# Optimization experiments

Measured on AMD Instinct MI355X. Metric: run time of the kernel, lower is better.

## Reference

```python
import jax, jax.numpy as jnp
import numpy as np

HALF = 16  # num_outputs // 2 with num_features = 32
EPS = 1e-5


def _gmul(Wm, h):
    # Wm: [B,N,M,J], h: [B,M,F] -> [B,N,J*F] (j-major feature layout, matching torch split/cat/bmm)
    B, N = Wm.shape[0], Wm.shape[1]
    return jnp.einsum('bnmj,bmf->bnjf', Wm, h).reshape(B, N, -1)


def _bn(z, g, b):
    # training-mode BatchNorm2d on [R, C, 1, 1] == per-channel norm over rows, biased var
    m = z.mean(axis=0)
    v = z.var(axis=0)
    return g * (z - m) / jnp.sqrt(v + EPS) + b


def _block(W, hx, W_lg, hy, P, wx2x, wy2x, bx, wy2y, wx2y, by, gx, btx, gy, bty):
    B, N, M = P.shape[0], P.shape[1], P.shape[2]
    x2x = _gmul(W, hx).reshape(-1, wx2x.shape[0])
    y2x = _gmul(P, hy).reshape(-1, wy2x.shape[0])
    zx = x2x @ wx2x + y2x @ wy2x + bx
    zx = jnp.concatenate([jax.nn.relu(zx[:, :HALF]), zx[:, HALF:]], axis=1)
    xo = _bn(zx, gx, btx).reshape(B, N, -1)
    y2y = _gmul(W_lg, hy).reshape(-1, wy2y.shape[0])
    x2y = _gmul(jnp.swapaxes(P, 1, 2), hx).reshape(-1, wx2y.shape[0])
    zy = y2y @ wy2y + x2y @ wx2y + by
    zy = jnp.concatenate([jax.nn.relu(zy[:, :HALF]), zy[:, HALF:]], axis=1)
    yo = _bn(zy, gy, bty).reshape(B, M, -1)
    return xo, yo


def _forward(W, x, W_lg, y, P,
             wx2x0, wy2x0, bx0, wy2y0, wx2y0, by0, gx0, btx0, gy0, bty0,
             wx2x_m, wy2x_m, bx_m, wy2y_m, wx2y_m, by_m, gx_m, btx_m, gy_m, bty_m,
             wlx, wly, bl):
    hx, hy = _block(W, x, W_lg, y, P, wx2x0, wy2x0, bx0, wy2y0, wx2y0, by0,
                    gx0, btx0, gy0, bty0)
    for i in range(wx2x_m.shape[0]):  # fixed num_layers loop
        hx, hy = _block(W, hx, W_lg, hy, P,
                        wx2x_m[i], wy2x_m[i], bx_m[i], wy2y_m[i], wx2y_m[i], by_m[i],
                        gx_m[i], btx_m[i], gy_m[i], bty_m[i])
    # final layer: linear only, x branch output
    x2x = _gmul(W, hx).reshape(-1, wlx.shape[0])
    y2x = _gmul(P, hy).reshape(-1, wly.shape[0])
    out = (x2x @ wlx + y2x @ wly + bl).reshape(W.shape[0], W.shape[1], -1)
    return out


def setup_inputs() -> dict:
    key = jax.random.key(0)
    ks = iter(jax.random.split(key, 40))
    B, N, M, J, F, L, C = 1, 2048, 4096, 3, 32, 6, 2
    d = {}
    d['W'] = jax.random.normal(next(ks), (B, N, N, J), jnp.float32)
    d['x'] = jax.random.normal(next(ks), (B, N, 1), jnp.float32)
    d['W_lg'] = jax.random.normal(next(ks), (B, M, M, J), jnp.float32)
    d['y'] = jax.random.normal(next(ks), (B, M, 1), jnp.float32)
    d['P'] = jax.random.normal(next(ks), (B, N, M, 2), jnp.float32)
    s = 0.1
    d['wx2x0'] = jax.random.normal(next(ks), (J * 1, F), jnp.float32) * s
    d['wy2x0'] = jax.random.normal(next(ks), (2 * 1, F), jnp.float32) * s
    d['bx0'] = jax.random.normal(next(ks), (F,), jnp.float32) * s
    d['wy2y0'] = jax.random.normal(next(ks), (J * 1, F), jnp.float32) * s
    d['wx2y0'] = jax.random.normal(next(ks), (2 * 1, F), jnp.float32) * s
    d['by0'] = jax.random.normal(next(ks), (F,), jnp.float32) * s
    d['gx0'] = jnp.ones((F,), jnp.float32)
    d['btx0'] = jnp.zeros((F,), jnp.float32)
    d['gy0'] = jnp.ones((F,), jnp.float32)
    d['bty0'] = jnp.zeros((F,), jnp.float32)
    d['wx2x_m'] = jax.random.normal(next(ks), (L, J * F, F), jnp.float32) * s
    d['wy2x_m'] = jax.random.normal(next(ks), (L, 2 * F, F), jnp.float32) * s
    d['bx_m'] = jax.random.normal(next(ks), (L, F), jnp.float32) * s
    d['wy2y_m'] = jax.random.normal(next(ks), (L, J * F, F), jnp.float32) * s
    d['wx2y_m'] = jax.random.normal(next(ks), (L, 2 * F, F), jnp.float32) * s
    d['by_m'] = jax.random.normal(next(ks), (L, F), jnp.float32) * s
    d['gx_m'] = jnp.ones((L, F), jnp.float32)
    d['btx_m'] = jnp.zeros((L, F), jnp.float32)
    d['gy_m'] = jnp.ones((L, F), jnp.float32)
    d['bty_m'] = jnp.zeros((L, F), jnp.float32)
    d['wlx'] = jax.random.normal(next(ks), (J * F, C), jnp.float32) * s
    d['wly'] = jax.random.normal(next(ks), (2 * F, C), jnp.float32) * s
    d['bl'] = jax.random.normal(next(ks), (C,), jnp.float32) * s
    return d


def reference(W, x, W_lg, y, P,
              wx2x0, wy2x0, bx0, wy2y0, wx2y0, by0, gx0, btx0, gy0, bty0,
              wx2x_m, wy2x_m, bx_m, wy2y_m, wx2y_m, by_m, gx_m, btx_m, gy_m, bty_m,
              wlx, wly, bl):
    return _forward(W, x, W_lg, y, P,
                    wx2x0, wy2x0, bx0, wy2y0, wx2y0, by0, gx0, btx0, gy0, bty0,
                    wx2x_m, wy2x_m, bx_m, wy2y_m, wx2y_m, by_m, gx_m, btx_m, gy_m, bty_m,
                    wlx, wly, bl)
```

## Files before the change

### kernel.cpp

```cpp
#include <hip/hip_runtime.h>

typedef _Float16 f16x8 __attribute__((ext_vector_type(8)));
typedef float f32x4 __attribute__((ext_vector_type(4)));


__device__ inline unsigned short f16b(float v) {
    _Float16 h = (_Float16)v;
    return __builtin_bit_cast(unsigned short, h);
}

__device__ inline void atomAddF(float* p, float v) {
    __hip_atomic_fetch_add(p, v, __ATOMIC_RELAXED, __HIP_MEMORY_SCOPE_AGENT);
}

template<int K>
__device__ inline void pack_cvt4(const float* __restrict__ src, unsigned short* __restrict__ dst, int q) {
    const int KSTEPS = K / 32;
    int r15 = q & 15;
    int blk = q >> 4;
    int panel = blk / KSTEPS;
    int kstep = blk - panel * KSTEPS;
    int row = (panel << 4) | r15;
    const float4* s = (const float4*)(src + (size_t)row * K + (kstep << 5));
    uint4* d = (uint4*)dst;
    #pragma unroll
    for (int g = 0; g < 4; ++g) {
        float4 v0 = s[g * 2], v1 = s[g * 2 + 1];
        uint4 qq;
        qq.x = (unsigned)f16b(v0.x) | ((unsigned)f16b(v0.y) << 16);
        qq.y = (unsigned)f16b(v0.z) | ((unsigned)f16b(v0.w) << 16);
        qq.z = (unsigned)f16b(v1.x) | ((unsigned)f16b(v1.y) << 16);
        qq.w = (unsigned)f16b(v1.z) | ((unsigned)f16b(v1.w) << 16);
        d[(size_t)blk * 64 + g * 16 + r15] = qq;
    }
}

__device__ inline void build_one(int t2,
    const float* __restrict__ srcx, const float* __restrict__ srcy,
    int Fin, int Fout, int buildB2, int use_bn,
    const float* __restrict__ stats,
    const float* __restrict__ w1a, const float* __restrict__ w1b,
    const float* __restrict__ w2a, const float* __restrict__ w2b,
    unsigned short* __restrict__ B1f, unsigned short* __restrict__ B2f) {
    const int NB1 = 14336 * 32;
    int isB2 = 0;
    if (t2 >= NB1) {
        if (!buildB2) return;
        isB2 = 1; t2 -= NB1;
        if (t2 >= 16384 * 32) return;
    }
    int g = t2 & 31;
    int k = t2 >> 5;
    float v = 0.f;
    if (g < Fout) {
        const float* hr; const float* wc; int useY;
        if (!isB2) {
            if (k < 6144) { int m = k / 3, j = k - 3 * m; hr = srcx + m * Fin; wc = w1a + (j * Fin) * Fout + g; useY = 0; }
            else { int k2 = k - 6144; int m = k2 >> 1, p = k2 & 1; hr = srcy + m * Fin; wc = w1b + (p * Fin) * Fout + g; useY = 1; }
        } else {
            if (k < 12288) { int m = k / 3, j = k - 3 * m; hr = srcy + m * Fin; wc = w2a + (j * Fin) * Fout + g; useY = 1; }
            else { int k2 = k - 12288; int n = k2 >> 1, p = k2 & 1; hr = srcx + n * Fin; wc = w2b + (p * Fin) * Fout + g; useY = 0; }
        }
        float a = 0.f;
        if (use_bn) {
            const float* sc = useY ? stats + 196 : stats + 132;
            const float* sh = useY ? stats + 228 : stats + 164;
            #pragma unroll
            for (int f = 0; f < 32; ++f) {
                float h = sc[f] * hr[f] + sh[f];
                a += h * wc[f * Fout];
            }
        } else {
            for (int f = 0; f < Fin; ++f) a += hr[f] * wc[f * Fout];
        }
        v = a;
    }
    int e = k & 7, kw = (k >> 3) & 3, t = k >> 5, hh = g >> 4;
    int off = (((t * 2 + hh) * 64 + (kw << 4) + (g & 15)) << 3) | e;
    if (!isB2) B1f[off] = f16b(v); else B2f[off] = f16b(v);
}

__global__ __launch_bounds__(256) void prep(const float* __restrict__ W, const float* __restrict__ WL,
                                            const float* __restrict__ P,
                                            const float* __restrict__ x, const float* __restrict__ y,
                                            const float* __restrict__ wx2x0, const float* __restrict__ wy2x0,
                                            const float* __restrict__ wy2y0, const float* __restrict__ wx2y0,
                                            unsigned short* __restrict__ Wb, unsigned short* __restrict__ WLb,
                                            unsigned short* __restrict__ Pb, unsigned short* __restrict__ PT,
                                            unsigned short* __restrict__ B1f, unsigned short* __restrict__ B2f) {
    __shared__ unsigned int lds[64][33];
    int bid = blockIdx.x;
    int tid = threadIdx.x;
    if (bid < 2048) {
        const int QW = 393216, QTOT = 393216 + 1572864;
        for (int q = bid * 256 + tid; q < QTOT; q += 2048 * 256) {
            if (q < QW) pack_cvt4<6144>(W, Wb, q);
            else pack_cvt4<12288>(WL, WLb, q - QW);
        }
        return;
    }
    if (bid >= 6144) {
        build_one((bid - 6144) * 256 + tid, x, y, 1, 32, 1, 0, nullptr,
                  wx2x0, wy2x0, wy2y0, wx2y0, B1f, B2f);
        return;
    }
    int vb = bid - 2048;
    int m0 = (vb & 127) * 32;
    int n0 = (vb >> 7) * 64;
    const float2* P2 = (const float2*)P;
    #pragma unroll
    for (int it = 0; it < 8; ++it) {
        int idx = it * 256 + tid;
        int nl = idx >> 5, ml = idx & 31;
        float2 v = P2[(size_t)(n0 + nl) * 4096 + (m0 + ml)];
        unsigned int pk = (unsigned int)f16b(v.x) | ((unsigned int)f16b(v.y) << 16);
        lds[nl][ml] = pk;
    }
    __syncthreads();
    uint4* PT4 = (uint4*)PT;
    uint4* Pb4 = (uint4*)Pb;
    #pragma unroll
    for (int it = 0; it < 2; ++it) {
        int t2 = it * 256 + tid;
        {
            int r15 = t2 & 15, kw = (t2 >> 4) & 3, ksi = (t2 >> 6) & 3, pi = t2 >> 8;
            int ml = pi * 16 + r15;
            int nl0 = ksi * 16 + kw * 4;
            uint4 u;
            u.x = lds[nl0][ml]; u.y = lds[nl0 + 1][ml]; u.z = lds[nl0 + 2][ml]; u.w = lds[nl0 + 3][ml];
            int rowp = (m0 >> 4) + pi;
            int ks = (n0 >> 4) + ksi;
            PT4[(size_t)rowp * 8192 + ks * 64 + kw * 16 + r15] = u;
        }
        {
            int r15 = t2 & 15, kw = (t2 >> 4) & 3, ksi = (t2 >> 6) & 1, pi = t2 >> 7;
            int nl = pi * 16 + r15;
            int ml0 = ksi * 16 + kw * 4;
            uint4 u;
            u.x = lds[nl][ml0]; u.y = lds[nl][ml0 + 1]; u.z = lds[nl][ml0 + 2]; u.w = lds[nl][ml0 + 3];
            int rowp = (n0 >> 4) + pi;
            int ks = (m0 >> 4) + ksi;
            Pb4[(size_t)rowp * 16384 + ks * 64 + kw * 16 + r15] = u;
        }
    }
}

__global__ __launch_bounds__(256) void build_b(
    const float* __restrict__ srcx, const float* __restrict__ srcy,
    int Fin, int Fout, int buildB2, int use_bn,
    const float* __restrict__ stats,
    const float* __restrict__ w1a, const float* __restrict__ w1b,
    const float* __restrict__ w2a, const float* __restrict__ w2b,
    unsigned short* __restrict__ B1f, unsigned short* __restrict__ B2f) {
    build_one(blockIdx.x * 256 + threadIdx.x, srcx, srcy, Fin, Fout, buildB2, use_bn,
              stats, w1a, w1b, w2a, w2b, B1f, B2f);
}

__global__ __launch_bounds__(256) void gemm_k(
    const unsigned short* __restrict__ Wb, const unsigned short* __restrict__ Pb,
    const unsigned short* __restrict__ WLb, const unsigned short* __restrict__ PTb,
    const unsigned short* __restrict__ B1f, const unsigned short* __restrict__ B2f,
    float* __restrict__ px, float* __restrict__ py, float* __restrict__ stats, int nwgx) {
    __shared__ float lds[4][1024];
    int bid = blockIdx.x;
    if (bid == 0 && threadIdx.x < 132) stats[threadIdx.x] = 0.f;
    const unsigned short* Bf;
    float* Z;
    int seg, Mbase, K, kloc, kb;
    const unsigned short* A16;
    if (bid < nwgx) {
        Bf = B1f;
        int mwg = bid / 14; seg = bid % 14;
        Mbase = mwg * 32;
        kb = seg << 10;
        Z = px + (size_t)seg * 65536;
        if (seg < 6) { K = 6144; kloc = kb;        A16 = Wb; }
        else         { K = 8192; kloc = kb - 6144; A16 = Pb; }
    } else {
        int b2 = bid - nwgx;
        Bf = B2f;
        int mwg = b2 / 16; seg = b2 % 16;
        Mbase = mwg * 32;
        kb = seg << 10;
        Z = py + (size_t)seg * 131072;
        if (seg < 12) { K = 12288; kloc = kb;         A16 = WLb; }
        else          { K = 4096;  kloc = kb - 12288; A16 = PTb; }
    }
    int wid = threadIdx.x >> 6, lane = threadIdx.x & 63;
    int kq = wid << 8;
    const unsigned short* ap0 = A16 + (size_t)(Mbase >> 4) * (K * 16)
                              + (size_t)((kloc + kq) >> 5) * 512 + lane * 8;
    const unsigned short* ap1 = ap0 + (size_t)K * 16;
    const unsigned short* bp = Bf + ((size_t)((kb + kq) >> 5)) * 1024 + lane * 8;
    f32x4 acc00 = {0.f,0.f,0.f,0.f}, acc01 = {0.f,0.f,0.f,0.f};
    f32x4 acc10 = {0.f,0.f,0.f,0.f}, acc11 = {0.f,0.f,0.f,0.f};
    #pragma unroll
    for (int ks = 0; ks < 8; ++ks) {
        f16x8 a0 = *(const f16x8*)ap0;
        f16x8 a1 = *(const f16x8*)ap1;
        f16x8 b0 = *(const f16x8*)bp;
        f16x8 b1 = *(const f16x8*)(bp + 512);
        acc00 = __builtin_amdgcn_mfma_f32_16x16x32_f16(a0, b0, acc00, 0, 0, 0);
        acc10 = __builtin_amdgcn_mfma_f32_16x16x32_f16(a1, b0, acc10, 0, 0, 0);
        acc01 = __builtin_amdgcn_mfma_f32_16x16x32_f16(a0, b1, acc01, 0, 0, 0);
        acc11 = __builtin_amdgcn_mfma_f32_16x16x32_f16(a1, b1, acc11, 0, 0, 0);
        ap0 += 512; ap1 += 512; bp += 1024;
    }
    int col = lane & 15, r0 = (lane >> 4) << 2;
    float* l = lds[wid];
    #pragma unroll
    for (int r = 0; r < 4; ++r) {
        l[(r0 + r) * 32 + col]            = acc00[r];
        l[(r0 + r) * 32 + col + 16]       = acc01[r];
        l[(r0 + r + 16) * 32 + col]       = acc10[r];
        l[(r0 + r + 16) * 32 + col + 16]  = acc11[r];
    }
    __syncthreads();
    int t = threadIdx.x;
    float4 a = ((const float4*)lds[0])[t];
    float4 b = ((const float4*)lds[1])[t];
    float4 c = ((const float4*)lds[2])[t];
    float4 d = ((const float4*)lds[3])[t];
    float4 s;
    s.x = (a.x + b.x) + (c.x + d.x);
    s.y = (a.y + b.y) + (c.y + d.y);
    s.z = (a.z + b.z) + (c.z + d.z);
    s.w = (a.w + b.w) + (c.w + d.w);
    ((float4*)(Z + (size_t)Mbase * 32))[t] = s;
}

__global__ __launch_bounds__(256) void reduce_stats(
    const float* __restrict__ px, const float* __restrict__ py,
    const float* __restrict__ bx, const float* __restrict__ by,
    const float* __restrict__ gx, const float* __restrict__ btx,
    const float* __restrict__ gy, const float* __restrict__ bty,
    float* __restrict__ zax, float* __restrict__ zay,
    float* __restrict__ stats) {
    __shared__ float lsum[4][8][8];
    __shared__ int lastFlag;
    int bid = blockIdx.x, tid = threadIdx.x;
    const float4* src; const float* bias; float4* dst; float* st; int nseg, i4, stride4;
    if (bid < 64) { src = (const float4*)px; bias = bx; dst = (float4*)zax; st = stats;      nseg = 14; i4 = bid * 256 + tid;        stride4 = 16384; }
    else          { src = (const float4*)py; bias = by; dst = (float4*)zay; st = stats + 64; nseg = 16; i4 = (bid - 64) * 256 + tid; stride4 = 32768; }
    float4 s = {0.f, 0.f, 0.f, 0.f};
    for (int g = 0; g < nseg; ++g) {
        float4 v = src[(size_t)g * stride4 + i4];
        s.x += v.x; s.y += v.y; s.z += v.z; s.w += v.w;
    }
    int c0 = (i4 & 7) * 4;
    float4 b4 = *(const float4*)(bias + c0);
    s.x += b4.x; s.y += b4.y; s.z += b4.z; s.w += b4.w;
    if (c0 < 16) {
        s.x = fmaxf(s.x, 0.f); s.y = fmaxf(s.y, 0.f);
        s.z = fmaxf(s.z, 0.f); s.w = fmaxf(s.w, 0.f);
    }
    dst[i4] = s;
    float4 s2 = {s.x * s.x, s.y * s.y, s.z * s.z, s.w * s.w};
    #pragma unroll
    for (int mask = 8; mask <= 32; mask <<= 1) {
        s.x += __shfl_xor(s.x, mask); s.y += __shfl_xor(s.y, mask);
        s.z += __shfl_xor(s.z, mask); s.w += __shfl_xor(s.w, mask);
        s2.x += __shfl_xor(s2.x, mask); s2.y += __shfl_xor(s2.y, mask);
        s2.z += __shfl_xor(s2.z, mask); s2.w += __shfl_xor(s2.w, mask);
    }
    int w = tid >> 6, ln = tid & 63;
    if (ln < 8) {
        lsum[w][ln][0] = s.x;  lsum[w][ln][1] = s.y;  lsum[w][ln][2] = s.z;  lsum[w][ln][3] = s.w;
        lsum[w][ln][4] = s2.x; lsum[w][ln][5] = s2.y; lsum[w][ln][6] = s2.z; lsum[w][ln][7] = s2.w;
    }
    __syncthreads();
    if (tid < 64) {
        int q = tid >> 3, e = tid & 7;
        float v = lsum[0][q][e] + lsum[1][q][e] + lsum[2][q][e] + lsum[3][q][e];
        int col = q * 4 + (e & 3);
        atomAddF((e < 4) ? &st[col] : &st[32 + col], v);
    }
    __syncthreads();
    if (tid == 0) {
        __threadfence();
        int old = __hip_atomic_fetch_add((int*)(stats + 128), 1, __ATOMIC_ACQ_REL, __HIP_MEMORY_SCOPE_AGENT);
        lastFlag = (old == 191) ? 1 : 0;
    }
    __syncthreads();
    if (lastFlag && tid < 64) {
        int f = tid & 31, isY = tid >> 5;
        float* sb = stats + (isY ? 64 : 0);
        float n = isY ? 4096.f : 2048.f;
        float sum = __hip_atomic_load(&sb[f], __ATOMIC_RELAXED, __HIP_MEMORY_SCOPE_AGENT);
        float ssq = __hip_atomic_load(&sb[32 + f], __ATOMIC_RELAXED, __HIP_MEMORY_SCOPE_AGENT);
        float mean = sum / n;
        float var = ssq / n - mean * mean;
        const float* gv = isY ? gy : gx;
        const float* bv = isY ? bty : btx;
        float sc = gv[f] * rsqrtf(var + 1e-5f);
        stats[132 + isY * 64 + f] = sc;
        stats[164 + isY * 64 + f] = bv[f] - mean * sc;
    }
}

__global__ __launch_bounds__(256) void out_final(const float* __restrict__ px,
                                                 const float* __restrict__ bl,
                                                 float* __restrict__ out) {
    int tid = blockIdx.x * 256 + threadIdx.x;
    if (tid < 4096) {
        int n = tid >> 1, c = tid & 1;
        float a = bl[c];
        for (int s = 0; s < 14; ++s) a += px[(size_t)s * 65536 + n * 32 + c];
        out[tid] = a;
    }
}

extern "C" void kernel_launch(void* const* d_in, const int* in_sizes, int n_in,
                              void* d_out, int out_size, void* d_ws, size_t ws_size,
                              hipStream_t stream) {
    const float* W    = (const float*)d_in[0];
    const float* x    = (const float*)d_in[1];
    const float* WL   = (const float*)d_in[2];
    const float* y    = (const float*)d_in[3];
    const float* P    = (const float*)d_in[4];
    const float* wx2x0 = (const float*)d_in[5];
    const float* wy2x0 = (const float*)d_in[6];
    const float* bx0   = (const float*)d_in[7];
    const float* wy2y0 = (const float*)d_in[8];
    const float* wx2y0 = (const float*)d_in[9];
    const float* by0   = (const float*)d_in[10];
    const float* gx0   = (const float*)d_in[11];
    const float* btx0  = (const float*)d_in[12];
    const float* gy0   = (const float*)d_in[13];
    const float* bty0  = (const float*)d_in[14];
    const float* wx2x_m = (const float*)d_in[15];
    const float* wy2x_m = (const float*)d_in[16];
    const float* bx_m   = (const float*)d_in[17];
    const float* wy2y_m = (const float*)d_in[18];
    const float* wx2y_m = (const float*)d_in[19];
    const float* by_m   = (const float*)d_in[20];
    const float* gx_m   = (const float*)d_in[21];
    const float* btx_m  = (const float*)d_in[22];
    const float* gy_m   = (const float*)d_in[23];
    const float* bty_m  = (const float*)d_in[24];
    const float* wlx = (const float*)d_in[25];
    const float* wly = (const float*)d_in[26];
    const float* bl  = (const float*)d_in[27];

    char* base = (char*)d_ws;
    unsigned short* Wb  = (unsigned short*)(base + 0);
    unsigned short* Pb  = (unsigned short*)(base + 25165824);
    unsigned short* WLb = (unsigned short*)(base + 58720256);
    unsigned short* PTb = (unsigned short*)(base + 159383552);
    unsigned short* B1f = (unsigned short*)(base + 192937984);
    unsigned short* B2f = (unsigned short*)(base + 193855488);
    float* zax   = (float*)(base + 194904064);
    float* zay   = (float*)(base + 195166208);
    float* stats = (float*)(base + 195690496);
    float* px    = (float*)(base + 195692544);
    float* py    = (float*)(base + 199362560);

    prep<<<9984, 256, 0, stream>>>(W, WL, P, x, y, wx2x0, wy2x0, wy2y0, wx2y0,
                                   Wb, WLb, Pb, PTb, B1f, B2f);

    gemm_k<<<2944, 256, 0, stream>>>(Wb, Pb, WLb, PTb, B1f, B2f, px, py, stats, 896);
    reduce_stats<<<192, 256, 0, stream>>>(px, py, bx0, by0, gx0, btx0, gy0, bty0, zax, zay, stats);

    for (int i = 0; i < 6; ++i) {
        build_b<<<3840, 256, 0, stream>>>(zax, zay, 32, 32, 1, 1, stats,
                                          wx2x_m + i * 3072, wy2x_m + i * 2048,
                                          wy2y_m + i * 3072, wx2y_m + i * 2048, B1f, B2f);
        gemm_k<<<2944, 256, 0, stream>>>(Wb, Pb, WLb, PTb, B1f, B2f, px, py, stats, 896);
        reduce_stats<<<192, 256, 0, stream>>>(px, py, bx_m + i * 32, by_m + i * 32,
                                              gx_m + i * 32, btx_m + i * 32,
                                              gy_m + i * 32, bty_m + i * 32, zax, zay, stats);
    }

    build_b<<<1792, 256, 0, stream>>>(zax, zay, 32, 2, 0, 1, stats,
                                      wlx, wly, nullptr, nullptr, B1f, B2f);
    gemm_k<<<896, 256, 0, stream>>>(Wb, Pb, WLb, PTb, B1f, B2f, px, py, stats, 896);
    out_final<<<16, 256, 0, stream>>>(px, bl, (float*)d_out);
}
```

Before: 602.7 us.

## Stage W/WL fp16 packing through LDS and software-pipeline GEMM operand loads

The fp32-to-fp16 packing of W and W_lg into MFMA panel layout now reads coalesced rows into a padded LDS tile, then writes packed 16-byte chunks. Previously each thread gathered strided 128-byte row segments. This targets uncoalesced global reads in the prep kernel, which streams the largest tensors. Separately, the GEMM inner loop now prefetches the next k-step's A/B fragments before issuing the current MFMAs, hiding load latency at the cost of extra registers.

```diff
diff --git a/kernel.cpp b/kernel.cpp
--- a/kernel.cpp
+++ b/kernel.cpp
@@ -2,7 +2,10 @@
 
 typedef _Float16 f16x8 __attribute__((ext_vector_type(8)));
 typedef float f32x4 __attribute__((ext_vector_type(4)));
-
+typedef unsigned short us4v __attribute__((ext_vector_type(4)));
+
+
+#define LPITCH 1036
 
 __device__ inline unsigned short f16b(float v) {
     _Float16 h = (_Float16)v;
@@ -14,24 +17,29 @@
 }
 
 template<int K>
-__device__ inline void pack_cvt4(const float* __restrict__ src, unsigned short* __restrict__ dst, int q) {
-    const int KSTEPS = K / 32;
-    int r15 = q & 15;
-    int blk = q >> 4;
-    int panel = blk / KSTEPS;
-    int kstep = blk - panel * KSTEPS;
-    int row = (panel << 4) | r15;
-    const float4* s = (const float4*)(src + (size_t)row * K + (kstep << 5));
-    uint4* d = (uint4*)dst;
-    #pragma unroll
-    for (int g = 0; g < 4; ++g) {
-        float4 v0 = s[g * 2], v1 = s[g * 2 + 1];
-        uint4 qq;
-        qq.x = (unsigned)f16b(v0.x) | ((unsigned)f16b(v0.y) << 16);
-        qq.y = (unsigned)f16b(v0.z) | ((unsigned)f16b(v0.w) << 16);
-        qq.z = (unsigned)f16b(v1.x) | ((unsigned)f16b(v1.y) << 16);
-        qq.w = (unsigned)f16b(v1.z) | ((unsigned)f16b(v1.w) << 16);
-        d[(size_t)blk * 64 + g * 16 + r15] = qq;
+__device__ inline void cvt_tile(const float* __restrict__ src, unsigned short* __restrict__ dst,
+                                int panel, int t0, unsigned short* lbuf) {
+    int tid = threadIdx.x;
+    int w = tid >> 6, lane = tid & 63;
+    const float* base = src + (size_t)(panel * 16) * K + t0 * 1024;
+    #pragma unroll 4
+    for (int i = 0; i < 16; ++i) {
+        float4 v = *((const float4*)(base + (size_t)i * K + w * 256) + lane);
+        us4v h;
+        h[0] = f16b(v.x); h[1] = f16b(v.y); h[2] = f16b(v.z); h[3] = f16b(v.w);
+        *(us4v*)(lbuf + i * LPITCH + w * 256 + lane * 4) = h;
+    }
+    __syncthreads();
+    uint4* d = (uint4*)dst + (size_t)panel * (K * 2) + t0 * 2048;
+    #pragma unroll
+    for (int j = 0; j < 8; ++j) {
+        int u = j * 256 + tid;
+        int r15 = u & 15, g = (u >> 4) & 3, ksl = u >> 6;
+        const unsigned short* p = lbuf + r15 * LPITCH + ksl * 32 + g * 8;
+        uint2 lo = *(const uint2*)p;
+        uint2 hi = *(const uint2*)(p + 4);
+        uint4 q; q.x = lo.x; q.y = lo.y; q.z = hi.x; q.w = hi.y;
+        d[u] = q;
     }
 }
 
@@ -88,23 +96,22 @@
                                             unsigned short* __restrict__ Wb, unsigned short* __restrict__ WLb,
                                             unsigned short* __restrict__ Pb, unsigned short* __restrict__ PT,
                                             unsigned short* __restrict__ B1f, unsigned short* __restrict__ B2f) {
-    __shared__ unsigned int lds[64][33];
+    __shared__ __align__(16) unsigned char smem[16 * LPITCH * 2];
     int bid = blockIdx.x;
     int tid = threadIdx.x;
-    if (bid < 2048) {
-        const int QW = 393216, QTOT = 393216 + 1572864;
-        for (int q = bid * 256 + tid; q < QTOT; q += 2048 * 256) {
-            if (q < QW) pack_cvt4<6144>(W, Wb, q);
-            else pack_cvt4<12288>(WL, WLb, q - QW);
-        }
+    if (bid < 3840) {
+        unsigned short* lbuf = (unsigned short*)smem;
+        if (bid < 768) cvt_tile<6144>(W, Wb, bid / 6, bid % 6, lbuf);
+        else { int b = bid - 768; cvt_tile<12288>(WL, WLb, b / 12, b % 12, lbuf); }
         return;
     }
-    if (bid >= 6144) {
-        build_one((bid - 6144) * 256 + tid, x, y, 1, 32, 1, 0, nullptr,
+    if (bid >= 7936) {
+        build_one((bid - 7936) * 256 + tid, x, y, 1, 32, 1, 0, nullptr,
                   wx2x0, wy2x0, wy2y0, wx2y0, B1f, B2f);
         return;
     }
-    int vb = bid - 2048;
+    unsigned int (*lds)[33] = (unsigned int (*)[33])smem;
+    int vb = bid - 3840;
     int m0 = (vb & 127) * 32;
     int n0 = (vb >> 7) * 64;
     const float2* P2 = (const float2*)P;
@@ -194,18 +201,27 @@
     const unsigned short* bp = Bf + ((size_t)((kb + kq) >> 5)) * 1024 + lane * 8;
     f32x4 acc00 = {0.f,0.f,0.f,0.f}, acc01 = {0.f,0.f,0.f,0.f};
     f32x4 acc10 = {0.f,0.f,0.f,0.f}, acc11 = {0.f,0.f,0.f,0.f};
-    #pragma unroll
-    for (int ks = 0; ks < 8; ++ks) {
-        f16x8 a0 = *(const f16x8*)ap0;
-        f16x8 a1 = *(const f16x8*)ap1;
-        f16x8 b0 = *(const f16x8*)bp;
-        f16x8 b1 = *(const f16x8*)(bp + 512);
+    f16x8 a0 = *(const f16x8*)ap0;
+    f16x8 a1 = *(const f16x8*)ap1;
+    f16x8 b0 = *(const f16x8*)bp;
+    f16x8 b1 = *(const f16x8*)(bp + 512);
+    #pragma unroll
+    for (int ks = 0; ks < 7; ++ks) {
+        ap0 += 512; ap1 += 512; bp += 1024;
+        f16x8 na0 = *(const f16x8*)ap0;
+        f16x8 na1 = *(const f16x8*)ap1;
+        f16x8 nb0 = *(const f16x8*)bp;
+        f16x8 nb1 = *(const f16x8*)(bp + 512);
         acc00 = __builtin_amdgcn_mfma_f32_16x16x32_f16(a0, b0, acc00, 0, 0, 0);
         acc10 = __builtin_amdgcn_mfma_f32_16x16x32_f16(a1, b0, acc10, 0, 0, 0);
         acc01 = __builtin_amdgcn_mfma_f32_16x16x32_f16(a0, b1, acc01, 0, 0, 0);
         acc11 = __builtin_amdgcn_mfma_f32_16x16x32_f16(a1, b1, acc11, 0, 0, 0);
-        ap0 += 512; ap1 += 512; bp += 1024;
-    }
+        a0 = na0; a1 = na1; b0 = nb0; b1 = nb1;
+    }
+    acc00 = __builtin_amdgcn_mfma_f32_16x16x32_f16(a0, b0, acc00, 0, 0, 0);
+    acc10 = __builtin_amdgcn_mfma_f32_16x16x32_f16(a1, b0, acc10, 0, 0, 0);
+    acc01 = __builtin_amdgcn_mfma_f32_16x16x32_f16(a0, b1, acc01, 0, 0, 0);
+    acc11 = __builtin_amdgcn_mfma_f32_16x16x32_f16(a1, b1, acc11, 0, 0, 0);
     int col = lane & 15, r0 = (lane >> 4) << 2;
     float* l = lds[wid];
     #pragma unroll
@@ -355,8 +371,8 @@
     float* px    = (float*)(base + 195692544);
     float* py    = (float*)(base + 199362560);
 
-    prep<<<9984, 256, 0, stream>>>(W, WL, P, x, y, wx2x0, wy2x0, wy2y0, wx2y0,
-                                   Wb, WLb, Pb, PTb, B1f, B2f);
+    prep<<<11776, 256, 0, stream>>>(W, WL, P, x, y, wx2x0, wy2x0, wy2y0, wx2y0,
+                                    Wb, WLb, Pb, PTb, B1f, B2f);
 
     gemm_k<<<2944, 256, 0, stream>>>(Wb, Pb, WLb, PTb, B1f, B2f, px, py, stats, 896);
     reduce_stats<<<192, 256, 0, stream>>>(px, py, bx0, by0, gx0, btx0, gy0, bty0, zax, zay, stats);
```

After: 590.0 us (median of 2 runs). -2.1%, faster.

## Split GEMM waves by row panel and K-half with register double-buffered loads

Applied to the files above, without the earlier changes.

Each workgroup's four waves are re-partitioned: instead of every wave covering both 16-row panels over a quarter of K, each wave now owns one row panel over half of K, running 16 k-steps with two accumulators instead of 8 steps with four. Global loads are double-buffered in registers so the next step's A/B fragments are fetched while the current MFMAs issue. The LDS reduction drops from a 4-way to a 2-way sum and the LDS footprint is halved. In exchange, each wave reloads B fragments that were previously shared across the two panels, which raises B traffic, and the per-wave dependency chain is longer.

```diff
diff --git a/kernel.cpp b/kernel.cpp
--- a/kernel.cpp
+++ b/kernel.cpp
@@ -161,7 +161,7 @@
     const unsigned short* __restrict__ WLb, const unsigned short* __restrict__ PTb,
     const unsigned short* __restrict__ B1f, const unsigned short* __restrict__ B2f,
     float* __restrict__ px, float* __restrict__ py, float* __restrict__ stats, int nwgx) {
-    __shared__ float lds[4][1024];
+    __shared__ float lds[4][512];
     int bid = blockIdx.x;
     if (bid == 0 && threadIdx.x < 132) stats[threadIdx.x] = 0.f;
     const unsigned short* Bf;
@@ -187,45 +187,46 @@
         else          { K = 4096;  kloc = kb - 12288; A16 = PTb; }
     }
     int wid = threadIdx.x >> 6, lane = threadIdx.x & 63;
-    int kq = wid << 8;
-    const unsigned short* ap0 = A16 + (size_t)(Mbase >> 4) * (K * 16)
-                              + (size_t)((kloc + kq) >> 5) * 512 + lane * 8;
-    const unsigned short* ap1 = ap0 + (size_t)K * 16;
-    const unsigned short* bp = Bf + ((size_t)((kb + kq) >> 5)) * 1024 + lane * 8;
-    f32x4 acc00 = {0.f,0.f,0.f,0.f}, acc01 = {0.f,0.f,0.f,0.f};
-    f32x4 acc10 = {0.f,0.f,0.f,0.f}, acc11 = {0.f,0.f,0.f,0.f};
-    #pragma unroll
-    for (int ks = 0; ks < 8; ++ks) {
-        f16x8 a0 = *(const f16x8*)ap0;
-        f16x8 a1 = *(const f16x8*)ap1;
-        f16x8 b0 = *(const f16x8*)bp;
-        f16x8 b1 = *(const f16x8*)(bp + 512);
-        acc00 = __builtin_amdgcn_mfma_f32_16x16x32_f16(a0, b0, acc00, 0, 0, 0);
-        acc10 = __builtin_amdgcn_mfma_f32_16x16x32_f16(a1, b0, acc10, 0, 0, 0);
-        acc01 = __builtin_amdgcn_mfma_f32_16x16x32_f16(a0, b1, acc01, 0, 0, 0);
-        acc11 = __builtin_amdgcn_mfma_f32_16x16x32_f16(a1, b1, acc11, 0, 0, 0);
-        ap0 += 512; ap1 += 512; bp += 1024;
+    int pw = wid & 1, kh = wid >> 1;
+    const unsigned short* ap = A16 + (size_t)((Mbase >> 4) + pw) * (K * 16)
+                             + (size_t)((kloc + kh * 512) >> 5) * 512 + lane * 8;
+    const unsigned short* bp = Bf + ((size_t)((kb + kh * 512) >> 5)) * 1024 + lane * 8;
+    f32x4 acc0 = {0.f,0.f,0.f,0.f}, acc1 = {0.f,0.f,0.f,0.f};
+    f16x8 A0 = *(const f16x8*)ap;
+    f16x8 P0 = *(const f16x8*)bp;
+    f16x8 Q0 = *(const f16x8*)(bp + 512);
+    ap += 512; bp += 1024;
+    f16x8 A1 = *(const f16x8*)ap;
+    f16x8 P1 = *(const f16x8*)bp;
+    f16x8 Q1 = *(const f16x8*)(bp + 512);
+    #pragma unroll
+    for (int ks = 0; ks < 16; ++ks) {
+        f16x8 a = (ks & 1) ? A1 : A0;
+        f16x8 b0 = (ks & 1) ? P1 : P0;
+        f16x8 b1 = (ks & 1) ? Q1 : Q0;
+        if (ks < 14) {
+            ap += 512; bp += 1024;
+            if (ks & 1) { A1 = *(const f16x8*)ap; P1 = *(const f16x8*)bp; Q1 = *(const f16x8*)(bp + 512); }
+            else        { A0 = *(const f16x8*)ap; P0 = *(const f16x8*)bp; Q0 = *(const f16x8*)(bp + 512); }
+        }
+        acc0 = __builtin_amdgcn_mfma_f32_16x16x32_f16(a, b0, acc0, 0, 0, 0);
+        acc1 = __builtin_amdgcn_mfma_f32_16x16x32_f16(a, b1, acc1, 0, 0, 0);
     }
     int col = lane & 15, r0 = (lane >> 4) << 2;
     float* l = lds[wid];
     #pragma unroll
     for (int r = 0; r < 4; ++r) {
-        l[(r0 + r) * 32 + col]            = acc00[r];
-        l[(r0 + r) * 32 + col + 16]       = acc01[r];
-        l[(r0 + r + 16) * 32 + col]       = acc10[r];
-        l[(r0 + r + 16) * 32 + col + 16]  = acc11[r];
+        l[(r0 + r) * 32 + col]      = acc0[r];
+        l[(r0 + r) * 32 + col + 16] = acc1[r];
     }
     __syncthreads();
     int t = threadIdx.x;
-    float4 a = ((const float4*)lds[0])[t];
-    float4 b = ((const float4*)lds[1])[t];
-    float4 c = ((const float4*)lds[2])[t];
-    float4 d = ((const float4*)lds[3])[t];
+    int r = t >> 3, c4 = t & 7;
+    int p = r >> 4, rl = r & 15;
+    float4 u = ((const float4*)lds[p])[rl * 8 + c4];
+    float4 v = ((const float4*)lds[2 + p])[rl * 8 + c4];
     float4 s;
-    s.x = (a.x + b.x) + (c.x + d.x);
-    s.y = (a.y + b.y) + (c.y + d.y);
-    s.z = (a.z + b.z) + (c.z + d.z);
-    s.w = (a.w + b.w) + (c.w + d.w);
+    s.x = u.x + v.x; s.y = u.y + v.y; s.z = u.z + v.z; s.w = u.w + v.w;
     ((float4*)(Z + (size_t)Mbase * 32))[t] = s;
 }
 
```

New measurement: 596.8 us. About the same (-1.0%).
